# Performance work log

Measured on AMD Instinct MI355X. Metric: run time of the kernel, lower is better.

Reference implementation:

```python
import jax, jax.numpy as jnp
import numpy as np

N_HEADS = 16
HEAD = 64
SEQ = 2048
EMBED = 1024
BATCH = 4

def setup_inputs() -> dict:
    key = jax.random.key(0)
    ks = jax.random.split(key, 6)
    inputs = jax.random.normal(ks[0], (BATCH, SEQ, EMBED), dtype=jnp.float32)
    # per-head projection weights stacked: [H, E, D] (nn.Linear(E, D, bias=False))
    s = 1.0 / np.sqrt(EMBED)
    Wq = jax.random.uniform(ks[1], (N_HEADS, EMBED, HEAD), jnp.float32, -s, s)
    Wk = jax.random.uniform(ks[2], (N_HEADS, EMBED, HEAD), jnp.float32, -s, s)
    Wv = jax.random.uniform(ks[3], (N_HEADS, EMBED, HEAD), jnp.float32, -s, s)
    Wo = jax.random.uniform(ks[4], (EMBED, EMBED), jnp.float32, -s, s)
    bo = jax.random.uniform(ks[5], (EMBED,), jnp.float32, -s, s)
    return {"inputs": inputs, "Wq": Wq, "Wk": Wk, "Wv": Wv, "Wo": Wo, "bo": bo}

def reference(inputs, Wq, Wk, Wv, Wo, bo):
    B, S, E = inputs.shape
    # batched per-head projections: [B,S,E] x [H,E,D] -> [B,H,S,D]
    q = jnp.einsum('bse,hed->bhsd', inputs, Wq)
    k = jnp.einsum('bse,hed->bhsd', inputs, Wk)
    v = jnp.einsum('bse,hed->bhsd', inputs, Wv)
    q = q / jnp.sqrt(jnp.float32(HEAD)).astype(q.dtype)
    scores = jnp.einsum('bhsd,bhtd->bhst', q, k)  # [B,H,S,S]
    causal = jnp.tril(jnp.ones((S, S), dtype=bool))
    scores = jnp.where(causal, scores, jnp.finfo(scores.dtype).min)
    weights = jax.nn.softmax(scores, axis=-1)
    out = jnp.einsum('bhst,bhtd->bhsd', weights, v)  # [B,H,S,D]
    # concat heads in head order -> [B,S,H*D]
    out = jnp.transpose(out, (0, 2, 1, 3)).reshape(B, S, N_HEADS * HEAD)
    return out @ Wo.T + bo
```

## Files before the change

kernel.cpp:

```cpp
#include <hip/hip_runtime.h>
#include <stdint.h>

typedef unsigned short ushort_t;
typedef __attribute__((ext_vector_type(8))) short short8;
typedef __attribute__((ext_vector_type(4))) short bf16x4;
typedef __attribute__((ext_vector_type(4))) float f32x4;

#define AS1 __attribute__((address_space(1)))
#define AS3 __attribute__((address_space(3)))

__device__ __forceinline__ void gl_lds16(const void* g, void* l) {
    __builtin_amdgcn_global_load_lds((const AS1 unsigned int*)g,
                                     (AS3 unsigned int*)l, 16, 0, 0);
}

__device__ __forceinline__ ushort_t f2bf(float f) {
    union { float f; unsigned u; } v; v.f = f;
    unsigned r = v.u + 0x7fffu + ((v.u >> 16) & 1u);
    return (ushort_t)(r >> 16);
}

__global__ __launch_bounds__(256) void prep_k(const float* __restrict__ inp,
                                              const float* __restrict__ Wo,
                                              const float* __restrict__ Wq,
                                              const float* __restrict__ Wk,
                                              const float* __restrict__ Wv,
                                              ushort_t* __restrict__ inp_bf,
                                              ushort_t* __restrict__ WoB,
                                              ushort_t* __restrict__ WT) {
    const int bx = blockIdx.x, tid = threadIdx.x;
    if (bx < 4608) {
        const float* src = (bx < 4096) ? inp : Wo;
        ushort_t* dst    = (bx < 4096) ? inp_bf : WoB;
        int i = ((bx < 4096 ? bx : bx - 4096) * 256 + tid) * 8;
        float4 a = *(const float4*)(src + i);
        float4 b = *(const float4*)(src + i + 4);
        short8 o;
        o[0] = (short)f2bf(a.x); o[1] = (short)f2bf(a.y);
        o[2] = (short)f2bf(a.z); o[3] = (short)f2bf(a.w);
        o[4] = (short)f2bf(b.x); o[5] = (short)f2bf(b.y);
        o[6] = (short)f2bf(b.z); o[7] = (short)f2bf(b.w);
        *(short8*)(dst + i) = o;
        return;
    }
    __shared__ ushort_t t[64 * 65];
    const int wb = bx - 4608;
    const int mat = wb >> 8;
    const int h   = (wb >> 4) & 15;
    const int et  = wb & 15;
    const float* W = (mat == 0 ? Wq : (mat == 1 ? Wk : Wv)) + h * (1024 * 64);
    const float* src = W + et * 64 * 64;
#pragma unroll
    for (int i = 0; i < 16; ++i) {
        int idx = i * 256 + tid;
        int e = idx >> 6, d = idx & 63;
        t[e * 65 + d] = f2bf(src[idx]);
    }
    __syncthreads();
    ushort_t* dst = WT + (mat * 16 + h) * (64 * 1024) + et * 64;
#pragma unroll
    for (int i = 0; i < 16; ++i) {
        int idx = i * 256 + tid;
        int d = idx >> 6, e = idx & 63;
        dst[d * 1024 + e] = t[e * 65 + d];
    }
}

__global__ __launch_bounds__(512, 4) void qkv_k(const ushort_t* __restrict__ A,
                                                const ushort_t* __restrict__ WT,
                                                ushort_t* __restrict__ Q,
                                                ushort_t* __restrict__ K,
                                                ushort_t* __restrict__ Vt) {
    __shared__ __align__(16) ushort_t ring[36864];
    const int tid = threadIdx.x, wave = tid >> 6, lane = tid & 63;
    const int ln15 = lane & 15, quad = lane >> 4;
    const int wm = wave >> 1, wn = wave & 1;
    const int m0 = blockIdx.x * 256, n0 = blockIdx.y * 128;

    const int sa_row  = wave * 16 + (lane >> 2);
    const int sa_colS = (((lane & 3) ^ ((lane >> 3) & 3))) * 8;
    const int woff    = wave * 512;
    const int rchunk  = (quad ^ ((ln15 >> 1) & 3)) * 8;

    f32x4 acc[4][4];
#pragma unroll
    for (int i = 0; i < 4; ++i)
#pragma unroll
        for (int j = 0; j < 4; ++j)
#pragma unroll
            for (int e = 0; e < 4; ++e) acc[i][j][e] = 0.f;

    auto stage = [&](int t, ushort_t* buf) {
        const int kb = t * 32;
        gl_lds16(A  + (size_t)(m0 + sa_row)       * 1024 + kb + sa_colS, buf + woff);
        gl_lds16(A  + (size_t)(m0 + 128 + sa_row) * 1024 + kb + sa_colS, buf + 4096 + woff);
        gl_lds16(WT + (size_t)(n0 + sa_row)       * 1024 + kb + sa_colS, buf + 8192 + woff);
    };

    stage(0, &ring[0]); stage(1, &ring[12288]);
    asm volatile("s_waitcnt vmcnt(3)" ::: "memory");
    __builtin_amdgcn_s_barrier();
    __builtin_amdgcn_sched_barrier(0);

    auto phase = [&](int t, const ushort_t* bufC, ushort_t* bufS) {
        short8 a[4], b[4];
#pragma unroll
        for (int f = 0; f < 4; ++f)
            a[f] = *(const short8*)&bufC[(wm * 64 + f * 16 + ln15) * 32 + rchunk];
#pragma unroll
        for (int f = 0; f < 4; ++f)
            b[f] = *(const short8*)&bufC[8192 + (wn * 64 + f * 16 + ln15) * 32 + rchunk];
        if (t + 2 < 32) stage(t + 2, bufS);
        if (t < 30)       asm volatile("s_waitcnt vmcnt(3)" ::: "memory");
        else if (t == 30) asm volatile("s_waitcnt vmcnt(0)" ::: "memory");
        __builtin_amdgcn_sched_barrier(0);
        __builtin_amdgcn_s_setprio(1);
#pragma unroll
        for (int fm = 0; fm < 4; ++fm)
#pragma unroll
            for (int fn = 0; fn < 4; ++fn)
                acc[fm][fn] = __builtin_amdgcn_mfma_f32_16x16x32_bf16(a[fm], b[fn], acc[fm][fn], 0, 0, 0);
        __builtin_amdgcn_s_setprio(0);
        __builtin_amdgcn_s_barrier();
        __builtin_amdgcn_sched_barrier(0);
    };

    for (int t3 = 0; t3 < 30; t3 += 3) {
        phase(t3,     &ring[0],     &ring[24576]);
        phase(t3 + 1, &ring[12288], &ring[0]);
        phase(t3 + 2, &ring[24576], &ring[12288]);
    }
    phase(30, &ring[0],     &ring[24576]);
    phase(31, &ring[12288], &ring[0]);

    const int n_base = n0 + wn * 64;
    const int mat = n_base >> 10;
    const int h   = (n_base >> 6) & 15;
    if (mat < 2) {
        ushort_t* dst = (mat == 0) ? Q : K;
        const float scale = (mat == 0) ? 0.125f : 1.0f;
#pragma unroll
        for (int fm = 0; fm < 4; ++fm) {
#pragma unroll
            for (int r = 0; r < 4; ++r) {
                int mg = m0 + wm * 64 + fm * 16 + quad * 4 + r;
                int bi = mg >> 11, s = mg & 2047;
                size_t base = ((size_t)(bi * 16 + h) * 2048 + s) * 64;
#pragma unroll
                for (int fn = 0; fn < 4; ++fn)
                    dst[base + fn * 16 + ln15] = f2bf(acc[fm][fn][r] * scale);
            }
        }
    } else {
        ushort_t* tb = &ring[wave * 4608];
#pragma unroll
        for (int fn = 0; fn < 4; ++fn)
#pragma unroll
            for (int fm = 0; fm < 4; ++fm) {
                bf16x4 pk;
#pragma unroll
                for (int r = 0; r < 4; ++r) pk[r] = (short)f2bf(acc[fm][fn][r]);
                *(bf16x4*)&tb[(fn * 16 + ln15) * 72 + fm * 16 + quad * 4] = pk;
            }
        const int s0 = m0 + wm * 64;
        const int bi = s0 >> 11, sb = s0 & 2047;
#pragma unroll
        for (int p = 0; p < 8; ++p) {
            int d  = p * 8 + (lane >> 3);
            int sc = (lane & 7) * 8;
            short8 vv = *(const short8*)&tb[d * 72 + sc];
            *(short8*)&Vt[((size_t)(bi * 16 + h) * 64 + d) * 2048 + sb + sc] = vv;
        }
    }
}

__global__ __launch_bounds__(256, 3) void flash_k(const ushort_t* Q, const ushort_t* K,
                                                  const ushort_t* Vt, ushort_t* Aout) {
    __shared__ __align__(16) ushort_t Ks[2][64 * 64];
    __shared__ __align__(16) ushort_t Vts[2][64 * 64];
    __shared__ __align__(16) ushort_t PT[4][32 * 72];
    const int tid = threadIdx.x, wave = tid >> 6, lane = tid & 63;
    const int ln15 = lane & 15, quad = lane >> 4;
    const int bx = blockIdx.x;
    const int qt = 15 - (bx >> 6);
    const int bh = bx & 63;
    const int qw = qt * 128 + wave * 32;
    const ushort_t* Kb = K + (size_t)bh * 2048 * 64;
    const ushort_t* Vb = Vt + (size_t)bh * 64 * 2048;
    ushort_t* myPT = PT[wave];
    const int srow = tid >> 3, c8 = (tid & 7) * 8;
    const int c8s  = ((tid & 7) ^ ((tid >> 3) & 7)) * 8;
    const int swr  = ln15 & 7;

    short8 qf[2][2];
    {
        const ushort_t* Qb = Q + (size_t)bh * 2048 * 64;
#pragma unroll
        for (int qs = 0; qs < 2; ++qs)
#pragma unroll
            for (int kk = 0; kk < 2; ++kk)
                qf[qs][kk] = *(const short8*)&Qb[(size_t)(qw + qs * 16 + ln15) * 64 + kk * 32 + quad * 8];
    }

    f32x4 o[4][2];
#pragma unroll
    for (int dt = 0; dt < 4; ++dt)
#pragma unroll
        for (int qs = 0; qs < 2; ++qs)
#pragma unroll
            for (int e = 0; e < 4; ++e) o[dt][qs][e] = 0.f;
    float l_s[2] = {0.f, 0.f};

    const int ktEnd = 2 * qt + 2;
    gl_lds16(Kb + (size_t)srow * 64 + c8s,        &Ks[0][srow * 64 + c8]);
    gl_lds16(Kb + (size_t)(32 + srow) * 64 + c8s, &Ks[0][(32 + srow) * 64 + c8]);
    gl_lds16(Vb + (size_t)srow * 2048 + c8s,        &Vts[0][srow * 64 + c8]);
    gl_lds16(Vb + (size_t)(32 + srow) * 2048 + c8s, &Vts[0][(32 + srow) * 64 + c8]);
    __syncthreads();

    for (int kt = 0; kt < ktEnd; ++kt) {
        const int cur = kt & 1, nxt = cur ^ 1;
        if (kt + 1 < ktEnd) {
            int kn = kt + 1;
            gl_lds16(Kb + (size_t)(kn * 64 + srow) * 64 + c8s,      &Ks[nxt][srow * 64 + c8]);
            gl_lds16(Kb + (size_t)(kn * 64 + 32 + srow) * 64 + c8s, &Ks[nxt][(32 + srow) * 64 + c8]);
            gl_lds16(Vb + (size_t)srow * 2048 + kn * 64 + c8s,        &Vts[nxt][srow * 64 + c8]);
            gl_lds16(Vb + (size_t)(32 + srow) * 2048 + kn * 64 + c8s, &Vts[nxt][(32 + srow) * 64 + c8]);
        }
        if (kt * 64 <= qw + 31) {
            f32x4 sc[4][2];
#pragma unroll
            for (int ks = 0; ks < 4; ++ks) {
#pragma unroll
                for (int qs = 0; qs < 2; ++qs)
#pragma unroll
                    for (int e = 0; e < 4; ++e) sc[ks][qs][e] = 0.f;
            }
            __builtin_amdgcn_s_setprio(1);
#pragma unroll
            for (int ks = 0; ks < 4; ++ks) {
#pragma unroll
                for (int kk = 0; kk < 2; ++kk) {
                    short8 kf = *(const short8*)&Ks[cur][(ks * 16 + ln15) * 64 + ((kk * 4 + quad) ^ swr) * 8];
#pragma unroll
                    for (int qs = 0; qs < 2; ++qs)
                        sc[ks][qs] = __builtin_amdgcn_mfma_f32_16x16x32_bf16(kf, qf[qs][kk], sc[ks][qs], 0, 0, 0);
                }
            }
            __builtin_amdgcn_s_setprio(0);
            if (kt * 64 + 63 > qw) {
#pragma unroll
                for (int ks = 0; ks < 4; ++ks)
#pragma unroll
                    for (int qs = 0; qs < 2; ++qs) {
                        int qg = qw + qs * 16 + ln15;
#pragma unroll
                        for (int r = 0; r < 4; ++r) {
                            int kg = kt * 64 + ks * 16 + quad * 4 + r;
                            if (kg > qg) sc[ks][qs][r] = -1e30f;
                        }
                    }
            }
#pragma unroll
            for (int qs = 0; qs < 2; ++qs) {
#pragma unroll
                for (int ks = 0; ks < 4; ++ks) {
                    bf16x4 pk;
#pragma unroll
                    for (int r = 0; r < 4; ++r) {
                        float p = __expf(sc[ks][qs][r]);
                        l_s[qs] += p;
                        pk[r] = (short)f2bf(p);
                    }
                    *(bf16x4*)&myPT[(qs * 16 + ln15) * 72 + ks * 16 + quad * 4] = pk;
                }
            }
            short8 pf[2][2];
#pragma unroll
            for (int qs = 0; qs < 2; ++qs)
#pragma unroll
                for (int kk = 0; kk < 2; ++kk)
                    pf[qs][kk] = *(const short8*)&myPT[(qs * 16 + ln15) * 72 + kk * 32 + quad * 8];
            __builtin_amdgcn_s_setprio(1);
#pragma unroll
            for (int dt = 0; dt < 4; ++dt)
#pragma unroll
                for (int kk = 0; kk < 2; ++kk) {
                    short8 vf = *(const short8*)&Vts[cur][(dt * 16 + ln15) * 64 + ((kk * 4 + quad) ^ swr) * 8];
#pragma unroll
                    for (int qs = 0; qs < 2; ++qs)
                        o[dt][qs] = __builtin_amdgcn_mfma_f32_16x16x32_bf16(vf, pf[qs][kk], o[dt][qs], 0, 0, 0);
                }
            __builtin_amdgcn_s_setprio(0);
        }
        __syncthreads();
    }
#pragma unroll
    for (int qs = 0; qs < 2; ++qs) {
        float l = l_s[qs];
        l += __shfl_xor(l, 16);
        l += __shfl_xor(l, 32);
        float inv = 1.f / l;
#pragma unroll
        for (int dt = 0; dt < 4; ++dt) {
            bf16x4 pk;
#pragma unroll
            for (int r = 0; r < 4; ++r) pk[r] = (short)f2bf(o[dt][qs][r] * inv);
            *(bf16x4*)&myPT[(qs * 16 + ln15) * 72 + dt * 16 + quad * 4] = pk;
        }
    }
    const int bi = bh >> 4, h = bh & 15;
#pragma unroll
    for (int p = 0; p < 4; ++p) {
        int row = p * 8 + (lane >> 3);
        int cc = (lane & 7) * 8;
        short8 vv = *(const short8*)&myPT[row * 72 + cc];
        int qg = qw + row;
        *(short8*)&Aout[((size_t)bi * 2048 + qg) * 1024 + h * 64 + cc] = vv;
    }
}

__global__ __launch_bounds__(256) void outproj_k(const ushort_t* A, const ushort_t* WoB,
                                                 const float* bo, float* Out) {
    __shared__ __align__(16) ushort_t As[2][128 * 64];
    __shared__ __align__(16) ushort_t Bs[2][128 * 64];
    const int tid = threadIdx.x, wave = tid >> 6, lane = tid & 63;
    const int ln15 = lane & 15, quad = lane >> 4;
    const int wm = wave >> 1, wn = wave & 1;
    const int lrow = lane >> 3, lcol = (lane & 7) * 8;
    const int lcolS = ((lane & 7) ^ (lane >> 3)) * 8;
    const int swr   = ln15 & 7;
    const int m0 = blockIdx.x * 128, n0 = blockIdx.y * 128;

    f32x4 acc[4][4];
#pragma unroll
    for (int i = 0; i < 4; ++i)
#pragma unroll
        for (int j = 0; j < 4; ++j)
#pragma unroll
            for (int e = 0; e < 4; ++e) acc[i][j][e] = 0.f;

#pragma unroll
    for (int i = 0; i < 4; ++i) {
        int br = i * 32 + wave * 8;
        gl_lds16(A   + (size_t)(m0 + br + lrow) * 1024 + lcolS, &As[0][br * 64]);
        gl_lds16(WoB + (size_t)(n0 + br + lrow) * 1024 + lcolS, &Bs[0][br * 64]);
    }
    __syncthreads();

    for (int it = 0; it < 16; ++it) {
        const int cur = it & 1, nxt = cur ^ 1;
        if (it < 15) {
            const int k0 = (it + 1) * 64;
#pragma unroll
            for (int i = 0; i < 4; ++i) {
                int br = i * 32 + wave * 8;
                gl_lds16(A   + (size_t)(m0 + br + lrow) * 1024 + k0 + lcolS, &As[nxt][br * 64]);
                gl_lds16(WoB + (size_t)(n0 + br + lrow) * 1024 + k0 + lcolS, &Bs[nxt][br * 64]);
            }
        }
#pragma unroll
        for (int kk = 0; kk < 2; ++kk) {
            short8 a[4], b[4];
#pragma unroll
            for (int f = 0; f < 4; ++f)
                a[f] = *(const short8*)&As[cur][(wm * 64 + f * 16 + ln15) * 64 + ((kk * 4 + quad) ^ swr) * 8];
#pragma unroll
            for (int f = 0; f < 4; ++f)
                b[f] = *(const short8*)&Bs[cur][(wn * 64 + f * 16 + ln15) * 64 + ((kk * 4 + quad) ^ swr) * 8];
#pragma unroll
            for (int fm = 0; fm < 4; ++fm)
#pragma unroll
                for (int fn = 0; fn < 4; ++fn)
                    acc[fm][fn] = __builtin_amdgcn_mfma_f32_16x16x32_bf16(a[fm], b[fn], acc[fm][fn], 0, 0, 0);
        }
        __syncthreads();
    }
#pragma unroll
    for (int fn = 0; fn < 4; ++fn) {
        int n = n0 + wn * 64 + fn * 16 + ln15;
        float bias = bo[n];
#pragma unroll
        for (int fm = 0; fm < 4; ++fm)
#pragma unroll
            for (int r = 0; r < 4; ++r) {
                int mg = m0 + wm * 64 + fm * 16 + quad * 4 + r;
                Out[(size_t)mg * 1024 + n] = acc[fm][fn][r] + bias;
            }
    }
}

extern "C" void kernel_launch(void* const* d_in, const int* in_sizes, int n_in,
                              void* d_out, int out_size, void* d_ws, size_t ws_size,
                              hipStream_t stream) {
    (void)in_sizes; (void)n_in; (void)out_size; (void)ws_size;
    const float* inp = (const float*)d_in[0];
    const float* Wq  = (const float*)d_in[1];
    const float* Wk  = (const float*)d_in[2];
    const float* Wv  = (const float*)d_in[3];
    const float* Wo  = (const float*)d_in[4];
    const float* bo  = (const float*)d_in[5];
    float* out = (float*)d_out;

    ushort_t* ws = (ushort_t*)d_ws;
    ushort_t* R0  = ws;
    ushort_t* WT  = R0  + 8388608;
    ushort_t* WoB = WT  + 3145728;
    ushort_t* Qb  = WoB + 1048576;
    ushort_t* Kb  = Qb  + 8388608;
    ushort_t* Vtb = Kb  + 8388608;

    ushort_t* inp_bf = R0;
    ushort_t* At     = R0;

    prep_k<<<5376, 256, 0, stream>>>(inp, Wo, Wq, Wk, Wv, inp_bf, WoB, WT);
    qkv_k<<<dim3(32, 24), 512, 0, stream>>>(inp_bf, WT, Qb, Kb, Vtb);
    flash_k<<<dim3(1024), 256, 0, stream>>>(Qb, Kb, Vtb, At);
    outproj_k<<<dim3(64, 8), 256, 0, stream>>>(At, WoB, bo, out);
}
```

Before: 226.1 us.

## Use packed bf16 conversion and triple-buffered 256x128 out-projection GEMM

Replaces the software round-to-nearest bf16 conversions in the V transpose, softmax probability store and flash epilogue with the hardware v_cvt_pk_bf16_f32 instruction. The out-projection kernel is restructured to 512 threads per 256x128 tile with a three-slot LDS ring over 32-wide K steps. Global-to-LDS loads are issued two stages ahead under explicit vmcnt waits and a single barrier per step. This aims to cut conversion ALU work and hide load latency in the final GEMM, at the cost of more LDS, hand-tuned waitcnt logic and fewer blocks.

```diff
diff --git a/kernel.cpp b/kernel.cpp
--- a/kernel.cpp
+++ b/kernel.cpp
@@ -18,6 +18,12 @@
     union { float f; unsigned u; } v; v.f = f;
     unsigned r = v.u + 0x7fffu + ((v.u >> 16) & 1u);
     return (ushort_t)(r >> 16);
+}
+
+__device__ __forceinline__ unsigned cvt_pk_bf16(float lo, float hi) {
+    unsigned r;
+    asm("v_cvt_pk_bf16_f32 %0, %1, %2" : "=v"(r) : "v"(lo), "v"(hi));
+    return r;
 }
 
 __global__ __launch_bounds__(256) void prep_k(const float* __restrict__ inp,
@@ -157,10 +163,10 @@
         for (int fn = 0; fn < 4; ++fn)
 #pragma unroll
             for (int fm = 0; fm < 4; ++fm) {
-                bf16x4 pk;
-#pragma unroll
-                for (int r = 0; r < 4; ++r) pk[r] = (short)f2bf(acc[fm][fn][r]);
-                *(bf16x4*)&tb[(fn * 16 + ln15) * 72 + fm * 16 + quad * 4] = pk;
+                uint2 w;
+                w.x = cvt_pk_bf16(acc[fm][fn][0], acc[fm][fn][1]);
+                w.y = cvt_pk_bf16(acc[fm][fn][2], acc[fm][fn][3]);
+                *(uint2*)&tb[(fn * 16 + ln15) * 72 + fm * 16 + quad * 4] = w;
             }
         const int s0 = m0 + wm * 64;
         const int bi = s0 >> 11, sb = s0 & 2047;
@@ -265,14 +271,15 @@
             for (int qs = 0; qs < 2; ++qs) {
 #pragma unroll
                 for (int ks = 0; ks < 4; ++ks) {
-                    bf16x4 pk;
-#pragma unroll
-                    for (int r = 0; r < 4; ++r) {
-                        float p = __expf(sc[ks][qs][r]);
-                        l_s[qs] += p;
-                        pk[r] = (short)f2bf(p);
-                    }
-                    *(bf16x4*)&myPT[(qs * 16 + ln15) * 72 + ks * 16 + quad * 4] = pk;
+                    float p0 = __expf(sc[ks][qs][0]);
+                    float p1 = __expf(sc[ks][qs][1]);
+                    float p2 = __expf(sc[ks][qs][2]);
+                    float p3 = __expf(sc[ks][qs][3]);
+                    l_s[qs] += (p0 + p1) + (p2 + p3);
+                    uint2 w;
+                    w.x = cvt_pk_bf16(p0, p1);
+                    w.y = cvt_pk_bf16(p2, p3);
+                    *(uint2*)&myPT[(qs * 16 + ln15) * 72 + ks * 16 + quad * 4] = w;
                 }
             }
             short8 pf[2][2];
@@ -303,10 +310,10 @@
         float inv = 1.f / l;
 #pragma unroll
         for (int dt = 0; dt < 4; ++dt) {
-            bf16x4 pk;
-#pragma unroll
-            for (int r = 0; r < 4; ++r) pk[r] = (short)f2bf(o[dt][qs][r] * inv);
-            *(bf16x4*)&myPT[(qs * 16 + ln15) * 72 + dt * 16 + quad * 4] = pk;
+            uint2 w;
+            w.x = cvt_pk_bf16(o[dt][qs][0] * inv, o[dt][qs][1] * inv);
+            w.y = cvt_pk_bf16(o[dt][qs][2] * inv, o[dt][qs][3] * inv);
+            *(uint2*)&myPT[(qs * 16 + ln15) * 72 + dt * 16 + quad * 4] = w;
         }
     }
     const int bi = bh >> 4, h = bh & 15;
@@ -320,17 +327,20 @@
     }
 }
 
-__global__ __launch_bounds__(256) void outproj_k(const ushort_t* A, const ushort_t* WoB,
-                                                 const float* bo, float* Out) {
-    __shared__ __align__(16) ushort_t As[2][128 * 64];
-    __shared__ __align__(16) ushort_t Bs[2][128 * 64];
+__global__ __launch_bounds__(512, 4) void outproj_k(const ushort_t* __restrict__ A,
+                                                    const ushort_t* __restrict__ WoB,
+                                                    const float* __restrict__ bo,
+                                                    float* __restrict__ Out) {
+    __shared__ __align__(16) ushort_t ring[36864];
     const int tid = threadIdx.x, wave = tid >> 6, lane = tid & 63;
     const int ln15 = lane & 15, quad = lane >> 4;
     const int wm = wave >> 1, wn = wave & 1;
-    const int lrow = lane >> 3, lcol = (lane & 7) * 8;
-    const int lcolS = ((lane & 7) ^ (lane >> 3)) * 8;
-    const int swr   = ln15 & 7;
-    const int m0 = blockIdx.x * 128, n0 = blockIdx.y * 128;
+    const int m0 = blockIdx.x * 256, n0 = blockIdx.y * 128;
+
+    const int sa_row  = wave * 16 + (lane >> 2);
+    const int sa_colS = (((lane & 3) ^ ((lane >> 3) & 3))) * 8;
+    const int woff    = wave * 512;
+    const int rchunk  = (quad ^ ((ln15 >> 1) & 3)) * 8;
 
     f32x4 acc[4][4];
 #pragma unroll
@@ -340,54 +350,62 @@
 #pragma unroll
             for (int e = 0; e < 4; ++e) acc[i][j][e] = 0.f;
 
-#pragma unroll
-    for (int i = 0; i < 4; ++i) {
-        int br = i * 32 + wave * 8;
-        gl_lds16(A   + (size_t)(m0 + br + lrow) * 1024 + lcolS, &As[0][br * 64]);
-        gl_lds16(WoB + (size_t)(n0 + br + lrow) * 1024 + lcolS, &Bs[0][br * 64]);
-    }
-    __syncthreads();
-
-    for (int it = 0; it < 16; ++it) {
-        const int cur = it & 1, nxt = cur ^ 1;
-        if (it < 15) {
-            const int k0 = (it + 1) * 64;
-#pragma unroll
-            for (int i = 0; i < 4; ++i) {
-                int br = i * 32 + wave * 8;
-                gl_lds16(A   + (size_t)(m0 + br + lrow) * 1024 + k0 + lcolS, &As[nxt][br * 64]);
-                gl_lds16(WoB + (size_t)(n0 + br + lrow) * 1024 + k0 + lcolS, &Bs[nxt][br * 64]);
-            }
-        }
-#pragma unroll
-        for (int kk = 0; kk < 2; ++kk) {
-            short8 a[4], b[4];
-#pragma unroll
-            for (int f = 0; f < 4; ++f)
-                a[f] = *(const short8*)&As[cur][(wm * 64 + f * 16 + ln15) * 64 + ((kk * 4 + quad) ^ swr) * 8];
-#pragma unroll
-            for (int f = 0; f < 4; ++f)
-                b[f] = *(const short8*)&Bs[cur][(wn * 64 + f * 16 + ln15) * 64 + ((kk * 4 + quad) ^ swr) * 8];
-#pragma unroll
-            for (int fm = 0; fm < 4; ++fm)
-#pragma unroll
-                for (int fn = 0; fn < 4; ++fn)
-                    acc[fm][fn] = __builtin_amdgcn_mfma_f32_16x16x32_bf16(a[fm], b[fn], acc[fm][fn], 0, 0, 0);
-        }
-        __syncthreads();
-    }
-#pragma unroll
-    for (int fn = 0; fn < 4; ++fn) {
-        int n = n0 + wn * 64 + fn * 16 + ln15;
-        float bias = bo[n];
+    auto stage = [&](int t, ushort_t* buf) {
+        const int kb = t * 32;
+        gl_lds16(A   + (size_t)(m0 + sa_row)       * 1024 + kb + sa_colS, buf + woff);
+        gl_lds16(A   + (size_t)(m0 + 128 + sa_row) * 1024 + kb + sa_colS, buf + 4096 + woff);
+        gl_lds16(WoB + (size_t)(n0 + sa_row)       * 1024 + kb + sa_colS, buf + 8192 + woff);
+    };
+
+    stage(0, &ring[0]); stage(1, &ring[12288]);
+    asm volatile("s_waitcnt vmcnt(3)" ::: "memory");
+    __builtin_amdgcn_s_barrier();
+    __builtin_amdgcn_sched_barrier(0);
+
+    auto phase = [&](int t, const ushort_t* bufC, ushort_t* bufS) {
+        short8 a[4], b[4];
+#pragma unroll
+        for (int f = 0; f < 4; ++f)
+            a[f] = *(const short8*)&bufC[(wm * 64 + f * 16 + ln15) * 32 + rchunk];
+#pragma unroll
+        for (int f = 0; f < 4; ++f)
+            b[f] = *(const short8*)&bufC[8192 + (wn * 64 + f * 16 + ln15) * 32 + rchunk];
+        if (t + 2 < 32) stage(t + 2, bufS);
+        if (t < 30)       asm volatile("s_waitcnt vmcnt(3)" ::: "memory");
+        else if (t == 30) asm volatile("s_waitcnt vmcnt(0)" ::: "memory");
+        __builtin_amdgcn_sched_barrier(0);
+        __builtin_amdgcn_s_setprio(1);
 #pragma unroll
         for (int fm = 0; fm < 4; ++fm)
 #pragma unroll
-            for (int r = 0; r < 4; ++r) {
-                int mg = m0 + wm * 64 + fm * 16 + quad * 4 + r;
-                Out[(size_t)mg * 1024 + n] = acc[fm][fn][r] + bias;
-            }
-    }
+            for (int fn = 0; fn < 4; ++fn)
+                acc[fm][fn] = __builtin_amdgcn_mfma_f32_16x16x32_bf16(a[fm], b[fn], acc[fm][fn], 0, 0, 0);
+        __builtin_amdgcn_s_setprio(0);
+        __builtin_amdgcn_s_barrier();
+        __builtin_amdgcn_sched_barrier(0);
+    };
+
+    for (int t3 = 0; t3 < 30; t3 += 3) {
+        phase(t3,     &ring[0],     &ring[24576]);
+        phase(t3 + 1, &ring[12288], &ring[0]);
+        phase(t3 + 2, &ring[24576], &ring[12288]);
+    }
+    phase(30, &ring[0],     &ring[24576]);
+    phase(31, &ring[12288], &ring[0]);
+
+    const int nb = n0 + wn * 64;
+    float bias[4];
+#pragma unroll
+    for (int fn = 0; fn < 4; ++fn) bias[fn] = bo[nb + fn * 16 + ln15];
+#pragma unroll
+    for (int fm = 0; fm < 4; ++fm)
+#pragma unroll
+        for (int r = 0; r < 4; ++r) {
+            int mg = m0 + wm * 64 + fm * 16 + quad * 4 + r;
+#pragma unroll
+            for (int fn = 0; fn < 4; ++fn)
+                Out[(size_t)mg * 1024 + nb + fn * 16 + ln15] = acc[fm][fn][r] + bias[fn];
+        }
 }
 
 extern "C" void kernel_launch(void* const* d_in, const int* in_sizes, int n_in,
@@ -416,5 +434,5 @@
     prep_k<<<5376, 256, 0, stream>>>(inp, Wo, Wq, Wk, Wv, inp_bf, WoB, WT);
     qkv_k<<<dim3(32, 24), 512, 0, stream>>>(inp_bf, WT, Qb, Kb, Vtb);
     flash_k<<<dim3(1024), 256, 0, stream>>>(Qb, Kb, Vtb, At);
-    outproj_k<<<dim3(64, 8), 256, 0, stream>>>(At, WoB, bo, out);
-}
+    outproj_k<<<dim3(32, 8), 512, 0, stream>>>(At, WoB, bo, out);
+}
```

Measured after the change: 216.5 us. 1.04x faster.
